# Kernel tuning notes

Measured on AMD Instinct MI355X. Metric: run time of the kernel, lower is better.

The kernel has to match this reference:

```python
import jax, jax.numpy as jnp
import numpy as np

B, C, H, W = 4, 512, 32, 32
NH = 8
HD = C // NH
PH, PW = 2, 4
NPR = PH * PW
HIDDEN = int(C * 2.0)
EPS = 1e-5

def _bn(x, p):
    g, b, m, v = p[0], p[1], p[2], p[3]
    s = g * jax.lax.rsqrt(v + EPS)
    return x * s[None, :, None, None] + (b - m * s)[None, :, None, None]

def _ln(x, p):
    mu = x.mean(-1, keepdims=True)
    var = ((x - mu) ** 2).mean(-1, keepdims=True)
    return (x - mu) * jax.lax.rsqrt(var + EPS) * p[0] + p[1]

def _dwconv(x, w):
    return jax.lax.conv_general_dilated(
        x, w, (1, 1), 'SAME',
        dimension_numbers=('NCHW', 'OIHW', 'NCHW'),
        feature_group_count=x.shape[1])

def _pw(x, w):
    # 1x1 conv, no bias: w is (O, I, 1, 1)
    return jnp.einsum('bchw,oc->bohw', x, w[:, :, 0, 0])

def _pool(x, ph, pw):
    # adaptive avg pool when output evenly divides input
    b, c, h, w = x.shape
    return x.reshape(b, c, ph, h // ph, pw, w // pw).mean(axis=(3, 5))

def _gelu(x):
    return jax.nn.gelu(x, approximate=False)

def _coords(h, w):
    y = jnp.linspace(0.0, 1.0, h)
    x = jnp.linspace(0.0, 1.0, w)
    gy, gx = jnp.meshgrid(y, x, indexing='ij')
    return jnp.stack([gy, gx], axis=-1).reshape(-1, 2)


def setup_inputs() -> dict:
    key = jax.random.key(0)
    ks = iter(jax.random.split(key, 64))
    def nrm(shape, s=0.02):
        return jax.random.normal(next(ks), shape, jnp.float32) * s
    def bnp():
        return jnp.stack([1.0 + nrm((C,), 0.1), nrm((C,), 0.1),
                          nrm((C,), 0.1), 1.0 + jnp.abs(nrm((C,), 0.2))])
    def lnp(c=C):
        return jnp.stack([jnp.ones((c,), jnp.float32), jnp.zeros((c,), jnp.float32)])
    return {
        'fused': jax.random.normal(next(ks), (B, C, H, W), jnp.float32),
        'depth': jax.random.normal(next(ks), (B, C, H, W), jnp.float32),
        'pg_dw_w': nrm((C, 1, 3, 3)), 'pg_bn1': bnp(),
        'pg_pw_w': nrm((C, C, 1, 1)), 'pg_bn2': bnp(),
        'prompt_embed': nrm((1, NPR, C)), 'pg_ln': lnp(),
        'gp_dw_w': nrm((C, 1, 3, 3)), 'gp_bn': bnp(),
        'gp_pw_w': nrm((1, C, 1, 1)), 'gp_pw_b': jnp.zeros((1,), jnp.float32),
        'gp_weight': jnp.ones((2, 1, 1, 1), jnp.float32),
        'ln1': lnp(),
        'wq': nrm((C, C)), 'wk': nrm((C, C)), 'wv': nrm((C, C)), 'wo': nrm((C, C)),
        'ln2': lnp(),
        'mlp_w1': nrm((HIDDEN, C)), 'mlp_b1': jnp.zeros((HIDDEN,), jnp.float32),
        'mlp_w2': nrm((C, HIDDEN)), 'mlp_b2': jnp.zeros((C,), jnp.float32),
        'op_dw_w': nrm((C, 1, 3, 3)), 'op_bn1': bnp(),
        'op_pw_w': nrm((C, C, 1, 1)), 'op_bn2': bnp(),
    }


def reference(fused, depth, pg_dw_w, pg_bn1, pg_pw_w, pg_bn2, prompt_embed, pg_ln,
              gp_dw_w, gp_bn, gp_pw_w, gp_pw_b, gp_weight,
              ln1, wq, wk, wv, wo, ln2, mlp_w1, mlp_b1, mlp_w2, mlp_b2,
              op_dw_w, op_bn1, op_pw_w, op_bn2):
    b = fused.shape[0]
    # --- DepthPromptGenerator ---
    pp = _gelu(_bn(_dwconv(depth, pg_dw_w), pg_bn1))
    pp = _gelu(_bn(_pw(pp, pg_pw_w), pg_bn2))
    prompt = _pool(pp, PH, PW).reshape(b, C, NPR).transpose(0, 2, 1)  # (B, P, C)
    prompt = _ln(prompt + prompt_embed, pg_ln)
    # --- GeometryPriorGenerator ---
    ds = _gelu(_bn(_dwconv(depth, gp_dw_w), gp_bn))
    ds = _pw(ds, gp_pw_w) + gp_pw_b[None, :, None, None]  # (B,1,H,W)
    img_d = ds.reshape(b, H * W)
    pr_d = _pool(ds, PH, PW).reshape(b, NPR)
    jd = jnp.concatenate([pr_d, img_d], axis=1)  # (B, N) depth scalar per token
    coords = jnp.concatenate([_coords(PH, PW), _coords(H, W)], axis=0)  # (N,2)
    pos = jnp.abs(coords[:, None, :] - coords[None, :, :]).sum(-1)  # (N,N) L1 distance
    decay = jnp.log(1.0 - 2.0 ** (-1.0 - 4.0 * jnp.arange(NH, dtype=jnp.float32) / NH))
    pos_mask = pos[None, :, :] * decay[:, None, None]  # (NH,N,N)
    depth_mask = jnp.abs(jd[:, :, None] - jd[:, None, :])[:, None, :, :] * decay[None, :, None, None]
    bias = gp_weight[0, 0, 0, 0] * pos_mask[None] + gp_weight[1, 0, 0, 0] * depth_mask  # (B,NH,N,N)
    # --- GeometryAwarePromptMixer ---
    img_tok = fused.reshape(b, C, H * W).transpose(0, 2, 1)  # (B,HW,C)
    jt = jnp.concatenate([prompt, img_tok], axis=1)  # (B,N,C)
    n = jt.shape[1]
    x = _ln(jt, ln1)
    q = jnp.einsum('bnc,dc->bnd', x, wq).reshape(b, n, NH, HD).transpose(0, 2, 1, 3)
    k = jnp.einsum('bnc,dc->bnd', x, wk).reshape(b, n, NH, HD).transpose(0, 2, 1, 3)
    v = jnp.einsum('bnc,dc->bnd', x, wv).reshape(b, n, NH, HD).transpose(0, 2, 1, 3)
    logits = jnp.einsum('bhnd,bhmd->bhnm', q, k) * (HD ** -0.5) + bias
    attn = jax.nn.softmax(logits, axis=-1)
    ao = jnp.einsum('bhnm,bhmd->bhnd', attn, v).transpose(0, 2, 1, 3).reshape(b, n, C)
    jt = jt + jnp.einsum('bnc,dc->bnd', ao, wo)
    h = _gelu(jnp.einsum('bnc,hc->bnh', _ln(jt, ln2), mlp_w1) + mlp_b1)
    jt = jt + jnp.einsum('bnh,ch->bnc', h, mlp_w2) + mlp_b2
    enh = jt[:, NPR:, :].transpose(0, 2, 1).reshape(b, C, H, W)
    # --- out_proj ---
    o = _gelu(_bn(_dwconv(enh, op_dw_w), op_bn1))
    o = _bn(_pw(o, op_pw_w), op_bn2)
    return fused + o
```

## Files before the change

### kernel.cpp

```cpp
#include <hip/hip_runtime.h>
#include <math.h>

typedef __attribute__((ext_vector_type(8))) short bf16x8;
typedef __attribute__((ext_vector_type(4))) float f32x4;

#define CH 512
#define HWP 1024
#define NTOK 1032
#define NTP 1088
#define NPRM 8
#define BB 4
#define EPSV 1e-5f
#define MTOK 4128
#define MPAD 4224
#define QSCL 0.18033688f
#define LOG2E 1.44269504f

__device__ __forceinline__ float gelu_f(float x) {
  return 0.5f * x * (1.0f + erff(x * 0.70710678118654752440f));
}

__device__ __forceinline__ ushort f2bf(float x) {
  union { float f; unsigned u; } v; v.f = x;
  unsigned r = v.u + 0x7FFF + ((v.u >> 16) & 1);
  return (ushort)(r >> 16);
}

__device__ __forceinline__ float bf2f(ushort u) {
  union { unsigned u; float f; } v; v.u = ((unsigned)u) << 16;
  return v.f;
}

__device__ __forceinline__ void gl16(const ushort* g, ushort* s) {
  __builtin_amdgcn_global_load_lds(
      (const __attribute__((address_space(1))) unsigned int*)g,
      (__attribute__((address_space(3))) unsigned int*)s,
      16, 0, 0);
}

__global__ __launch_bounds__(256) void convw(
    const float* __restrict__ wq, const float* __restrict__ wk, const float* __restrict__ wv,
    const float* __restrict__ wo, const float* __restrict__ w1, const float* __restrict__ w2,
    const float* __restrict__ pgw, const float* __restrict__ opw, const float* __restrict__ gpw,
    ushort* __restrict__ out)
{
  const int total = 2621952;
  for (int i = blockIdx.x * 256 + threadIdx.x; i < total; i += gridDim.x * 256) {
    const float* src; int off;
    if (i < 262144)       { src = wq;  off = i; }
    else if (i < 524288)  { src = wk;  off = i - 262144; }
    else if (i < 786432)  { src = wv;  off = i - 524288; }
    else if (i < 1048576) { src = wo;  off = i - 786432; }
    else if (i < 1572864) { src = w1;  off = i - 1048576; }
    else if (i < 2097152) { src = w2;  off = i - 1572864; }
    else if (i < 2359296) { src = pgw; off = i - 2097152; }
    else if (i < 2621440) { src = opw; off = i - 2359296; }
    else                  { src = gpw; off = i - 2621440; }
    out[i] = f2bf(src[off]);
  }
}

__global__ __launch_bounds__(256) void dwt_dual(
    const float* __restrict__ in,
    const float* __restrict__ w1p, const float* __restrict__ bn1,
    const float* __restrict__ w2p, const float* __restrict__ bn2,
    ushort* __restrict__ o1, ushort* __restrict__ o2)
{
  __shared__ float t1[32][33];
  __shared__ float t2[32][33];
  const int y = blockIdx.x;
  const int c0 = blockIdx.y * 32;
  const int b = blockIdx.z;
  const int tx = threadIdx.x, ty = threadIdx.y;
  #pragma unroll
  for (int i = 0; i < 4; ++i) {
    int c = c0 + ty + i * 8;
    const float* ip = in + ((size_t)(b * CH + c)) * HWP;
    const float* wa = w1p + c * 9;
    const float* wb = w2p + c * 9;
    float a1 = 0.0f, a2 = 0.0f;
    #pragma unroll
    for (int dy = 0; dy < 3; ++dy) {
      int yy = y + dy - 1;
      if ((unsigned)yy < 32u) {
        #pragma unroll
        for (int dx = 0; dx < 3; ++dx) {
          int xx = tx + dx - 1;
          if ((unsigned)xx < 32u) {
            float v = ip[yy * 32 + xx];
            a1 += v * wa[dy * 3 + dx];
            a2 += v * wb[dy * 3 + dx];
          }
        }
      }
    }
    float g1 = bn1[c], be1 = bn1[CH + c], m1 = bn1[2 * CH + c], v1 = bn1[3 * CH + c];
    float s1 = g1 * rsqrtf(v1 + EPSV);
    t1[ty + i * 8][tx] = gelu_f(a1 * s1 + (be1 - m1 * s1));
    float g2 = bn2[c], be2 = bn2[CH + c], m2 = bn2[2 * CH + c], v2 = bn2[3 * CH + c];
    float s2 = g2 * rsqrtf(v2 + EPSV);
    t2[ty + i * 8][tx] = gelu_f(a2 * s2 + (be2 - m2 * s2));
  }
  __syncthreads();
  #pragma unroll
  for (int i = 0; i < 4; ++i) {
    size_t row = (size_t)(b * HWP + y * 32 + ty + i * 8) * CH + c0 + tx;
    o1[row] = f2bf(t1[tx][ty + i * 8]);
    o2[row] = f2bf(t2[tx][ty + i * 8]);
  }
}

template<int KH>
__device__ __forceinline__ void g64_core(
    const ushort* __restrict__ Ab, const ushort* __restrict__ Bb,
    int KA, int KB, ushort* sA, ushort* sB,
    f32x4 (&acc)[2][2], int l, int w)
{
  const int wr = (w >> 1) * 32, wc = (w & 1) * 32;
  #pragma unroll
  for (int kh = 0; kh < KH; ++kh) {
    if (kh) __syncthreads();
    #pragma unroll
    for (int j = 0; j < 8; ++j) {
      int r2 = w * 16 + j * 2;
      int row = r2 + (l >> 5);
      int chk = (l & 31) ^ (row & 7);
      gl16(Ab + (size_t)row * KA + kh * 256 + chk * 8, sA + r2 * 256);
      gl16(Bb + (size_t)row * KB + kh * 256 + chk * 8, sB + r2 * 256);
    }
    __syncthreads();
    #pragma unroll
    for (int kt = 0; kt < 8; ++kt) {
      int q = kt * 4 + (l >> 4);
      int r0 = wr + (l & 15), r1 = wr + 16 + (l & 15);
      int c0i = wc + (l & 15), c1i = wc + 16 + (l & 15);
      bf16x8 a0 = *(const bf16x8*)(sA + r0 * 256 + ((q ^ (r0 & 7)) * 8));
      bf16x8 a1 = *(const bf16x8*)(sA + r1 * 256 + ((q ^ (r1 & 7)) * 8));
      bf16x8 b0 = *(const bf16x8*)(sB + c0i * 256 + ((q ^ (c0i & 7)) * 8));
      bf16x8 b1 = *(const bf16x8*)(sB + c1i * 256 + ((q ^ (c1i & 7)) * 8));
      acc[0][0] = __builtin_amdgcn_mfma_f32_16x16x32_bf16(a0, b0, acc[0][0], 0, 0, 0);
      acc[0][1] = __builtin_amdgcn_mfma_f32_16x16x32_bf16(a0, b1, acc[0][1], 0, 0, 0);
      acc[1][0] = __builtin_amdgcn_mfma_f32_16x16x32_bf16(a1, b0, acc[1][0], 0, 0, 0);
      acc[1][1] = __builtin_amdgcn_mfma_f32_16x16x32_bf16(a1, b1, acc[1][1], 0, 0, 0);
    }
  }
}

#define G64_PRE(Abase, Bbase, KAv, KBv, KHv) \
  __shared__ ushort sA[16384], sB[16384]; \
  f32x4 acc[2][2]; \
  { f32x4 z = {0.f, 0.f, 0.f, 0.f}; acc[0][0] = z; acc[0][1] = z; acc[1][0] = z; acc[1][1] = z; } \
  const int l = threadIdx.x & 63, w = threadIdx.x >> 6; \
  const int wr = (w >> 1) * 32, wc = (w & 1) * 32; \
  g64_core<KHv>((Abase), (Bbase), (KAv), (KBv), sA, sB, acc, l, w);

__global__ __launch_bounds__(256) void g_qkv(
    const ushort* __restrict__ A, const ushort* __restrict__ B,
    ushort* __restrict__ qh, ushort* __restrict__ kh, ushort* __restrict__ vt)
{
  const int n0 = blockIdx.x * 64, m0 = blockIdx.y * 64;
  G64_PRE(A + (size_t)m0 * 512, B + (size_t)n0 * 512, 512, 512, 2)
  #pragma unroll
  for (int nf = 0; nf < 2; ++nf) {
    int n = n0 + wc + nf * 16 + (l & 15);
    #pragma unroll
    for (int mf = 0; mf < 2; ++mf) {
      #pragma unroll
      for (int r = 0; r < 4; ++r) {
        int m = m0 + wr + mf * 16 + (l >> 4) * 4 + r;
        if (m < MTOK) {
          int b = m / NTOK;
          int tok = m - b * NTOK;
          float val = acc[mf][nf][r];
          if (n < 512) {
            qh[((size_t)((b * 8 + (n >> 6)) * NTP) + tok) * 64 + (n & 63)] = f2bf(val * QSCL);
          } else if (n < 1024) {
            int n2 = n - 512;
            kh[((size_t)((b * 8 + (n2 >> 6)) * NTP) + tok) * 64 + (n2 & 63)] = f2bf(val);
          } else {
            int n2 = n - 1024;
            vt[((size_t)((b * 8 + (n2 >> 6)) * 64) + (n2 & 63)) * NTP + tok] = f2bf(val);
          }
        }
      }
    }
  }
}

template<int KH>
__global__ __launch_bounds__(256) void g_res(
    const ushort* __restrict__ A, const ushort* __restrict__ B,
    float* __restrict__ Cf, const float* __restrict__ bias)
{
  const int n0 = blockIdx.x * 64, m0 = blockIdx.y * 64;
  G64_PRE(A + (size_t)m0 * (KH * 256), B + (size_t)n0 * (KH * 256), KH * 256, KH * 256, KH)
  #pragma unroll
  for (int nf = 0; nf < 2; ++nf) {
    int n = n0 + wc + nf * 16 + (l & 15);
    float bv = bias ? bias[n] : 0.0f;
    #pragma unroll
    for (int mf = 0; mf < 2; ++mf) {
      #pragma unroll
      for (int r = 0; r < 4; ++r) {
        int m = m0 + wr + mf * 16 + (l >> 4) * 4 + r;
        if (m < MTOK) Cf[(size_t)m * 512 + n] += acc[mf][nf][r] + bv;
      }
    }
  }
}

__global__ __launch_bounds__(256) void g_gelu(
    const ushort* __restrict__ A, const ushort* __restrict__ B,
    const float* __restrict__ bias, ushort* __restrict__ Ob)
{
  const int n0 = blockIdx.x * 64, m0 = blockIdx.y * 64;
  G64_PRE(A + (size_t)m0 * 512, B + (size_t)n0 * 512, 512, 512, 2)
  #pragma unroll
  for (int nf = 0; nf < 2; ++nf) {
    int n = n0 + wc + nf * 16 + (l & 15);
    float bv = bias[n];
    #pragma unroll
    for (int mf = 0; mf < 2; ++mf) {
      #pragma unroll
      for (int r = 0; r < 4; ++r) {
        int m = m0 + wr + mf * 16 + (l >> 4) * 4 + r;
        if (m < MTOK) Ob[(size_t)m * 1024 + n] = f2bf(gelu_f(acc[mf][nf][r] + bv));
      }
    }
  }
}

__global__ __launch_bounds__(256) void g_pw_pool(
    const ushort* __restrict__ A, const ushort* __restrict__ B,
    const float* __restrict__ bnp, float* __restrict__ ppool)
{
  __shared__ float poolL[8][64];
  const int hw0 = blockIdx.x * 64, m0 = blockIdx.y * 64;
  const int b = blockIdx.z;
  {
    int t = threadIdx.x;
    #pragma unroll
    for (int k = 0; k < 2; ++k) { int idx = t + k * 256; poolL[idx >> 6][idx & 63] = 0.0f; }
  }
  G64_PRE(A + (size_t)m0 * 512, B + (size_t)(b * HWP + hw0) * 512, 512, 512, 2)
  __syncthreads();
  #pragma unroll
  for (int mf = 0; mf < 2; ++mf) {
    #pragma unroll
    for (int r = 0; r < 4; ++r) {
      int ol = wr + mf * 16 + (l >> 4) * 4 + r;
      int o = m0 + ol;
      float g = bnp[o], be = bnp[CH + o], mm = bnp[2 * CH + o], vv = bnp[3 * CH + o];
      float s = g * rsqrtf(vv + EPSV);
      float sh = be - mm * s;
      #pragma unroll
      for (int nf = 0; nf < 2; ++nf) {
        int hw = hw0 + wc + nf * 16 + (l & 15);
        float x = gelu_f(acc[mf][nf][r] * s + sh);
        int y = hw >> 5, xx = hw & 31;
        int rg = (y >> 4) * 4 + (xx >> 3);
        atomicAdd(&poolL[rg][ol], x);
      }
    }
  }
  __syncthreads();
  {
    int t = threadIdx.x;
    #pragma unroll
    for (int k = 0; k < 2; ++k) {
      int idx = t + k * 256;
      int rg = idx >> 6, oo = idx & 63;
      float v = poolL[rg][oo];
      if (v != 0.0f)
        atomicAdd(&ppool[((size_t)(b * 8 + rg)) * 512 + m0 + oo], v * (1.0f / 128.0f));
    }
  }
}

__global__ __launch_bounds__(256) void g_pw_res(
    const ushort* __restrict__ A, const ushort* __restrict__ B,
    const float* __restrict__ bnp, const float* __restrict__ res, float* __restrict__ Of)
{
  const int hw0 = blockIdx.x * 64, m0 = blockIdx.y * 64;
  const int b = blockIdx.z;
  G64_PRE(A + (size_t)m0 * 512, B + (size_t)(b * HWP + hw0) * 512, 512, 512, 2)
  #pragma unroll
  for (int mf = 0; mf < 2; ++mf) {
    #pragma unroll
    for (int r = 0; r < 4; ++r) {
      int o = m0 + wr + mf * 16 + (l >> 4) * 4 + r;
      float g = bnp[o], be = bnp[CH + o], mm = bnp[2 * CH + o], vv = bnp[3 * CH + o];
      float s = g * rsqrtf(vv + EPSV);
      float sh = be - mm * s;
      #pragma unroll
      for (int nf = 0; nf < 2; ++nf) {
        int hw = hw0 + wc + nf * 16 + (l & 15);
        size_t oi = ((size_t)(b * CH + o)) * HWP + hw;
        Of[oi] = acc[mf][nf][r] * s + sh + res[oi];
      }
    }
  }
}

__global__ __launch_bounds__(256) void combo_mid(
    const float* __restrict__ fused, const float* __restrict__ ppool,
    const float* __restrict__ embed, const float* __restrict__ pgln,
    const float* __restrict__ ln1, float* __restrict__ jt, ushort* __restrict__ xb,
    const ushort* __restrict__ dwT2, const ushort* __restrict__ gpw,
    const float* __restrict__ b0, float* __restrict__ jdv)
{
  __shared__ float T[32][513];
  __shared__ float red[16];
  const int t = threadIdx.x;
  const int bx = blockIdx.x;
  if (bx < 128) {
    int b = bx >> 5, hw0 = (bx & 31) * 32;
    int tx = t & 31, ty = t >> 5;
    #pragma unroll
    for (int cc = 0; cc < 512; cc += 8)
      T[tx][cc + ty] = fused[((size_t)(b * 512 + cc + ty)) * 1024 + hw0 + tx];
    __syncthreads();
    int tok = t >> 3, j = t & 7;
    float s = 0.f, sq = 0.f;
    #pragma unroll
    for (int i = 0; i < 64; ++i) {
      float v = T[tok][j * 64 + i];
      s += v; sq += v * v;
    }
    s += __shfl_xor(s, 1); sq += __shfl_xor(sq, 1);
    s += __shfl_xor(s, 2); sq += __shfl_xor(sq, 2);
    s += __shfl_xor(s, 4); sq += __shfl_xor(sq, 4);
    float mu = s * (1.f / 512.f);
    float var = sq * (1.f / 512.f) - mu * mu;
    float rstd = rsqrtf(var + EPSV);
    size_t row = (size_t)(b * NTOK + NPRM + hw0 + tok);
    #pragma unroll
    for (int i = 0; i < 64; i += 4) {
      int c = j * 64 + i;
      float4 v4;
      v4.x = T[tok][c]; v4.y = T[tok][c + 1]; v4.z = T[tok][c + 2]; v4.w = T[tok][c + 3];
      *(float4*)(jt + row * 512 + c) = v4;
      ushort4 u;
      u.x = f2bf((v4.x - mu) * rstd * ln1[c] + ln1[512 + c]);
      u.y = f2bf((v4.y - mu) * rstd * ln1[c + 1] + ln1[512 + c + 1]);
      u.z = f2bf((v4.z - mu) * rstd * ln1[c + 2] + ln1[512 + c + 2]);
      u.w = f2bf((v4.w - mu) * rstd * ln1[c + 3] + ln1[512 + c + 3]);
      *(ushort4*)(xb + row * 512 + c) = u;
    }
  } else if (bx < 160) {
    int idx = bx - 128, b = idx >> 3, pI = idx & 7;
    int c = t * 2;
    float2 v = *(const float2*)(ppool + ((size_t)(b * 8 + pI)) * 512 + c);
    float2 e = *(const float2*)(embed + pI * 512 + c);
    v.x += e.x; v.y += e.y;
    float s = v.x + v.y, sq = v.x * v.x + v.y * v.y;
    #pragma unroll
    for (int off = 1; off < 64; off <<= 1) { s += __shfl_xor(s, off); sq += __shfl_xor(sq, off); }
    if ((t & 63) == 0) { red[(t >> 6) * 2] = s; red[(t >> 6) * 2 + 1] = sq; }
    __syncthreads();
    s = red[0] + red[2] + red[4] + red[6];
    sq = red[1] + red[3] + red[5] + red[7];
    float mu = s * (1.f / 512.f);
    float rstd = rsqrtf(sq * (1.f / 512.f) - mu * mu + EPSV);
    float o0 = (v.x - mu) * rstd * pgln[c] + pgln[512 + c];
    float o1 = (v.y - mu) * rstd * pgln[c + 1] + pgln[512 + c + 1];
    size_t row = (size_t)(b * NTOK + pI);
    jt[row * 512 + c] = o0;
    jt[row * 512 + c + 1] = o1;
    float s2 = o0 + o1, sq2 = o0 * o0 + o1 * o1;
    #pragma unroll
    for (int off = 1; off < 64; off <<= 1) { s2 += __shfl_xor(s2, off); sq2 += __shfl_xor(sq2, off); }
    if ((t & 63) == 0) { red[8 + (t >> 6) * 2] = s2; red[9 + (t >> 6) * 2] = sq2; }
    __syncthreads();
    s2 = red[8] + red[10] + red[12] + red[14];
    sq2 = red[9] + red[11] + red[13] + red[15];
    float mu2 = s2 * (1.f / 512.f);
    float rstd2 = rsqrtf(sq2 * (1.f / 512.f) - mu2 * mu2 + EPSV);
    xb[row * 512 + c]     = f2bf((o0 - mu2) * rstd2 * ln1[c] + ln1[512 + c]);
    xb[row * 512 + c + 1] = f2bf((o1 - mu2) * rstd2 * ln1[c + 1] + ln1[512 + c + 1]);
  } else {
    int idx = bx - 160;
    int b = idx >> 6, row0 = (idx & 63) * 16;
    int l = t & 63, w = t >> 6;
    bf16x8 wv = *(const bf16x8*)(gpw + l * 8);
    float wf[8];
    #pragma unroll
    for (int j = 0; j < 8; ++j) wf[j] = bf2f((ushort)wv[j]);
    float bias0 = b0[0];
    #pragma unroll
    for (int rr = 0; rr < 4; ++rr) {
      int hw = row0 + w * 4 + rr;
      bf16x8 xv = *(const bf16x8*)(dwT2 + ((size_t)(b * HWP + hw)) * CH + l * 8);
      float s = 0.0f;
      #pragma unroll
      for (int j = 0; j < 8; ++j) s += wf[j] * bf2f((ushort)xv[j]);
      #pragma unroll
      for (int off = 1; off < 64; off <<= 1) s += __shfl_xor(s, off);
      if (l == 0) {
        float sf = s + bias0;
        jdv[b * NTP + NPRM + hw] = sf;
        int y = hw >> 5, xx = hw & 31;
        int rg = (y >> 4) * 4 + (xx >> 3);
        atomicAdd(&jdv[b * NTP + rg], sf * (1.0f / 128.0f));
      }
    }
  }
}

__global__ __launch_bounds__(128) void ln_rows_bf(
    const float* __restrict__ in, const float* __restrict__ lnp, ushort* __restrict__ out)
{
  int row = blockIdx.x;
  float4 val = ((const float4*)(in + (size_t)row * CH))[threadIdx.x];
  float sum = val.x + val.y + val.z + val.w;
  float sq = val.x * val.x + val.y * val.y + val.z * val.z + val.w * val.w;
  #pragma unroll
  for (int off = 1; off < 64; off <<= 1) { sum += __shfl_xor(sum, off); sq += __shfl_xor(sq, off); }
  __shared__ float s2[4];
  if ((threadIdx.x & 63) == 0) { s2[(threadIdx.x >> 6) * 2] = sum; s2[(threadIdx.x >> 6) * 2 + 1] = sq; }
  __syncthreads();
  sum = s2[0] + s2[2]; sq = s2[1] + s2[3];
  float mu = sum * (1.0f / 512.0f);
  float var = sq * (1.0f / 512.0f) - mu * mu;
  float rstd = rsqrtf(var + EPSV);
  int c = threadIdx.x * 4;
  ushort4 o;
  o.x = f2bf((val.x - mu) * rstd * lnp[c] + lnp[CH + c]);
  o.y = f2bf((val.y - mu) * rstd * lnp[c + 1] + lnp[CH + c + 1]);
  o.z = f2bf((val.z - mu) * rstd * lnp[c + 2] + lnp[CH + c + 2]);
  o.w = f2bf((val.w - mu) * rstd * lnp[c + 3] + lnp[CH + c + 3]);
  *(ushort4*)(out + (size_t)row * CH + c) = o;
}

__global__ __launch_bounds__(256) void dwt_op(
    const float* __restrict__ jt, const float* __restrict__ w9p,
    const float* __restrict__ bn, ushort* __restrict__ outT)
{
  __shared__ float Tt[3][32][33];
  const int y = blockIdx.x;
  const int c0 = blockIdx.y * 32;
  const int b = blockIdx.z;
  const int tx = threadIdx.x, ty = threadIdx.y;
  #pragma unroll
  for (int ry = 0; ry < 3; ++ry) {
    int yy = y - 1 + ry;
    bool ok = (unsigned)yy < 32u;
    #pragma unroll
    for (int it = 0; it < 4; ++it) {
      int px = ty + it * 8;
      float v = ok ? jt[((size_t)(b * NTOK + NPRM + yy * 32 + px)) * 512 + c0 + tx] : 0.0f;
      Tt[ry][px][tx] = v;
    }
  }
  __syncthreads();
  int c = c0 + tx;
  float w9[9];
  #pragma unroll
  for (int k = 0; k < 9; ++k) w9[k] = w9p[c * 9 + k];
  float g = bn[c], be = bn[CH + c], mm = bn[2 * CH + c], vv = bn[3 * CH + c];
  float s = g * rsqrtf(vv + EPSV);
  float sh = be - mm * s;
  #pragma unroll
  for (int it = 0; it < 4; ++it) {
    int px = ty + it * 8;
    float acc = 0.0f;
    #pragma unroll
    for (int dy = 0; dy < 3; ++dy) {
      #pragma unroll
      for (int dx = 0; dx < 3; ++dx) {
        int xx = px + dx - 1;
        if ((unsigned)xx < 32u) acc += Tt[dy][xx][tx] * w9[dy * 3 + dx];
      }
    }
    outT[((size_t)(b * HWP + y * 32 + px)) * CH + c] = f2bf(gelu_f(acc * s + sh));
  }
}

__device__ __forceinline__ void tok_coord(int idx, float& y, float& x)
{
  if (idx < NPRM) { y = (float)(idx >> 2); x = (float)(idx & 3) * (1.0f / 3.0f); }
  else { int t = idx - NPRM; y = (float)(t >> 5) * (1.0f / 31.0f); x = (float)(t & 31) * (1.0f / 31.0f); }
}

__global__ __launch_bounds__(256) void attn_mfma3(
    const ushort* __restrict__ qh, const ushort* __restrict__ kh,
    const ushort* __restrict__ vT, const float* __restrict__ jd,
    const float* __restrict__ gw, ushort* __restrict__ ao)
{
  __shared__ ushort sK[8192], sV[8192];
  __shared__ ushort Pl[4][16][72];
  __shared__ float jdL[NTP];
  const int t = threadIdx.x, l = t & 63, w = t >> 6;
  const int h = blockIdx.y, b = blockIdx.z;
  const int i0 = blockIdx.x * 64 + w * 16;
  const ushort* Q = qh + (size_t)(b * 8 + h) * NTP * 64;
  const ushort* K = kh + (size_t)(b * 8 + h) * NTP * 64;
  const ushort* V = vT + (size_t)(b * 8 + h) * 64 * NTP;
  const float decay = logf(1.0f - exp2f(-1.0f - 0.5f * (float)h)) * LOG2E;
  const float g0 = gw[0] * decay, g1 = gw[1] * decay;

  for (int i = t; i < NTP; i += 256) jdL[i] = jd[b * NTP + i];

  bf16x8 qf0 = *(const bf16x8*)(Q + (size_t)(i0 + (l & 15)) * 64 + (l >> 4) * 8);
  bf16x8 qf1 = *(const bf16x8*)(Q + (size_t)(i0 + (l & 15)) * 64 + 32 + (l >> 4) * 8);

  bf16x8 ones;
  {
    short ov = (short)((l & 15) == 0 ? 0x3F80 : 0);
    #pragma unroll
    for (int j = 0; j < 8; ++j) ones[j] = ov;
  }

  f32x4 of[4], lacc;
  { f32x4 z = {0.f, 0.f, 0.f, 0.f};
    #pragma unroll
    for (int d = 0; d < 4; ++d) of[d] = z;
    lacc = z; }

#define ASTAGE(buf, j0s) { \
    const ushort* gk = K + (size_t)((j0s) + l) * 64; \
    const ushort* gv = V + (size_t)l * NTP + (j0s); \
    gl16(gk + w * 8,       sK + (buf) * 4096 + w * 512); \
    gl16(gk + (w + 4) * 8, sK + (buf) * 4096 + (w + 4) * 512); \
    gl16(gv + w * 8,       sV + (buf) * 4096 + w * 512); \
    gl16(gv + (w + 4) * 8, sV + (buf) * 4096 + (w + 4) * 512); }

  ASTAGE(0, 0)
  __syncthreads();

  float yi[4], xi[4], jdi[4];
  #pragma unroll
  for (int r = 0; r < 4; ++r) {
    int i = i0 + (l >> 4) * 4 + r;
    tok_coord(i, yi[r], xi[r]);
    jdi[r] = jdL[i];
  }

  const int NJT = 17;
  for (int jti = 0; jti < NJT; ++jti) {
    const int j0 = jti * 64;
    if (jti + 1 < NJT) ASTAGE((jti + 1) & 1, j0 + 64)
    const ushort* bK = sK + (jti & 1) * 4096;
    const ushort* bV = sV + (jti & 1) * 4096;

    f32x4 sfr[4];
    __builtin_amdgcn_s_setprio(1);
    #pragma unroll
    for (int jf = 0; jf < 4; ++jf) {
      bf16x8 k0 = *(const bf16x8*)(bK + (((l >> 4)) * 64 + jf * 16 + (l & 15)) * 8);
      bf16x8 k1 = *(const bf16x8*)(bK + ((4 + (l >> 4)) * 64 + jf * 16 + (l & 15)) * 8);
      f32x4 z = {0.f, 0.f, 0.f, 0.f};
      z = __builtin_amdgcn_mfma_f32_16x16x32_bf16(qf0, k0, z, 0, 0, 0);
      z = __builtin_amdgcn_mfma_f32_16x16x32_bf16(qf1, k1, z, 0, 0, 0);
      sfr[jf] = z;
    }
    __builtin_amdgcn_s_setprio(0);
    #pragma unroll
    for (int jf = 0; jf < 4; ++jf) {
      int jj = j0 + jf * 16 + (l & 15);
      float yj, xj;
      tok_coord(jj, yj, xj);
      float jdj = jdL[jj];
      bool valid = jj < NTOK;
      #pragma unroll
      for (int r = 0; r < 4; ++r) {
        float bias = g0 * (fabsf(yi[r] - yj) + fabsf(xi[r] - xj)) + g1 * fabsf(jdi[r] - jdj);
        float p = valid ? exp2f(sfr[jf][r] + bias - 4.0f) : 0.0f;
        Pl[w][(l >> 4) * 4 + r][jf * 16 + (l & 15)] = f2bf(p);
      }
    }
    asm volatile("s_waitcnt lgkmcnt(0)" ::: "memory");
    bf16x8 pa0 = *(const bf16x8*)&Pl[w][l & 15][(l >> 4) * 8];
    bf16x8 pa1 = *(const bf16x8*)&Pl[w][l & 15][32 + (l >> 4) * 8];
    __builtin_amdgcn_s_setprio(1);
    #pragma unroll
    for (int df = 0; df < 4; ++df) {
      bf16x8 v0 = *(const bf16x8*)(bV + (((l >> 4)) * 64 + df * 16 + (l & 15)) * 8);
      bf16x8 v1 = *(const bf16x8*)(bV + ((4 + (l >> 4)) * 64 + df * 16 + (l & 15)) * 8);
      of[df] = __builtin_amdgcn_mfma_f32_16x16x32_bf16(pa0, v0, of[df], 0, 0, 0);
      of[df] = __builtin_amdgcn_mfma_f32_16x16x32_bf16(pa1, v1, of[df], 0, 0, 0);
    }
    lacc = __builtin_amdgcn_mfma_f32_16x16x32_bf16(pa0, ones, lacc, 0, 0, 0);
    lacc = __builtin_amdgcn_mfma_f32_16x16x32_bf16(pa1, ones, lacc, 0, 0, 0);
    __builtin_amdgcn_s_setprio(0);
    __syncthreads();
  }
  #pragma unroll
  for (int r = 0; r < 4; ++r) {
    int i = i0 + (l >> 4) * 4 + r;
    float lsum = __shfl(lacc[r], (l & 48), 64);
    if (i < NTOK) {
      float inv = 1.0f / lsum;
      #pragma unroll
      for (int df = 0; df < 4; ++df)
        ao[((size_t)(b * NTOK + i)) * 512 + h * 64 + df * 16 + (l & 15)] = f2bf(of[df][r] * inv);
    }
  }
}

extern "C" void kernel_launch(void* const* d_in, const int* in_sizes, int n_in,
                              void* d_out, int out_size, void* d_ws, size_t ws_size,
                              hipStream_t stream)
{
  const float* fused = (const float*)d_in[0];
  const float* depth = (const float*)d_in[1];
  const float* pg_dw_w = (const float*)d_in[2];
  const float* pg_bn1 = (const float*)d_in[3];
  const float* pg_pw_w = (const float*)d_in[4];
  const float* pg_bn2 = (const float*)d_in[5];
  const float* prompt_embed = (const float*)d_in[6];
  const float* pg_ln = (const float*)d_in[7];
  const float* gp_dw_w = (const float*)d_in[8];
  const float* gp_bn = (const float*)d_in[9];
  const float* gp_pw_w = (const float*)d_in[10];
  const float* gp_pw_b = (const float*)d_in[11];
  const float* gp_weight = (const float*)d_in[12];
  const float* ln1 = (const float*)d_in[13];
  const float* wq = (const float*)d_in[14];
  const float* wk = (const float*)d_in[15];
  const float* wv = (const float*)d_in[16];
  const float* wo = (const float*)d_in[17];
  const float* ln2 = (const float*)d_in[18];
  const float* mlp_w1 = (const float*)d_in[19];
  const float* mlp_b1 = (const float*)d_in[20];
  const float* mlp_w2 = (const float*)d_in[21];
  const float* mlp_b2 = (const float*)d_in[22];
  const float* op_dw_w = (const float*)d_in[23];
  const float* op_bn1 = (const float*)d_in[24];
  const float* op_pw_w = (const float*)d_in[25];
  const float* op_bn2 = (const float*)d_in[26];
  float* out = (float*)d_out;

  char* p = (char*)d_ws;
  auto alloc = [&](size_t bytes) { char* r = p; p += (bytes + 1023) & ~(size_t)1023; return r; };
  float*  jdv   = (float*) alloc((size_t)BB * NTP * 4);
  float*  ppool = (float*) alloc((size_t)BB * 8 * CH * 4);
  float*  jt    = (float*) alloc((size_t)MTOK * 512 * 4);
  ushort* xb    = (ushort*)alloc((size_t)MPAD * 512 * 2);
  ushort* hb    = (ushort*)alloc((size_t)MPAD * 1024 * 2);
  ushort* ao    = (ushort*)alloc((size_t)MPAD * 512 * 2);
  ushort* qhB   = (ushort*)alloc((size_t)32 * NTP * 64 * 2);
  ushort* khB   = (ushort*)alloc((size_t)32 * NTP * 64 * 2);
  ushort* vTB   = (ushort*)alloc((size_t)32 * NTP * 64 * 2);
  ushort* dwT1  = (ushort*)alloc((size_t)BB * HWP * CH * 2);
  ushort* dwT2  = (ushort*)alloc((size_t)BB * HWP * CH * 2);
  ushort* wbf   = (ushort*)alloc((size_t)2621952 * 2);

  ushort* wqkv_bf = wbf;
  ushort* wo_bf   = wbf + 786432;
  ushort* w1_bf   = wbf + 1048576;
  ushort* w2_bf   = wbf + 1572864;
  ushort* pgw_bf  = wbf + 2097152;
  ushort* opw_bf  = wbf + 2359296;
  ushort* gpw_bf  = wbf + 2621440;

  hipMemsetAsync(jdv, 0, (size_t)BB * NTP * 4, stream);
  hipMemsetAsync(ppool, 0, (size_t)BB * 8 * CH * 4, stream);

  hipLaunchKernelGGL(convw, dim3(2048), dim3(256), 0, stream,
                     wq, wk, wv, wo, mlp_w1, mlp_w2, pg_pw_w, op_pw_w, gp_pw_w, wbf);

  hipLaunchKernelGGL(dwt_dual, dim3(32, 16, BB), dim3(32, 8), 0, stream,
                     depth, pg_dw_w, pg_bn1, gp_dw_w, gp_bn, dwT1, dwT2);
  hipLaunchKernelGGL(g_pw_pool, dim3(16, 8, BB), dim3(256), 0, stream, pgw_bf, dwT1, pg_bn2, ppool);
  hipLaunchKernelGGL(combo_mid, dim3(416), dim3(256), 0, stream,
                     fused, ppool, prompt_embed, pg_ln, ln1, jt, xb, dwT2, gpw_bf, gp_pw_b, jdv);
  hipLaunchKernelGGL(g_qkv, dim3(24, 65), dim3(256), 0, stream, xb, wqkv_bf, qhB, khB, vTB);
  hipLaunchKernelGGL(attn_mfma3, dim3(17, 8, BB), dim3(256), 0, stream, qhB, khB, vTB, jdv, gp_weight, ao);
  hipLaunchKernelGGL(g_res<2>, dim3(8, 65), dim3(256), 0, stream, ao, wo_bf, jt, (const float*)nullptr);
  hipLaunchKernelGGL(ln_rows_bf, dim3(MTOK), dim3(128), 0, stream, jt, ln2, xb);
  hipLaunchKernelGGL(g_gelu, dim3(16, 65), dim3(256), 0, stream, xb, w1_bf, mlp_b1, hb);
  hipLaunchKernelGGL(g_res<4>, dim3(8, 65), dim3(256), 0, stream, hb, w2_bf, jt, mlp_b2);
  hipLaunchKernelGGL(dwt_op, dim3(32, 16, BB), dim3(32, 8), 0, stream, jt, op_dw_w, op_bn1, dwT1);
  hipLaunchKernelGGL(g_pw_res, dim3(16, 8, BB), dim3(256), 0, stream, opw_bf, dwT1, op_bn2, fused, out);
}
```

Before: 331.6 us.

## Widen attention blocks to 128 queries, swizzle K/V LDS, split V transpose

The attention kernel now runs 512 threads per block covering 128 query rows, so each staged K/V tile is shared by twice as many waves. The K/V shared-memory layout is XOR-swizzled to avoid LDS bank conflicts, and the per-batch depth values are read from global memory instead of an LDS copy. The QKV GEMM now writes V in row-major head layout with coalesced stores, and a separate tiled transpose kernel produces V transposed. The token padding grows to a multiple of 128 to fit the new tiling. The cost is an extra launch, an extra V buffer and a round trip through memory for V.

```diff
diff --git a/kernel.cpp b/kernel.cpp
--- a/kernel.cpp
+++ b/kernel.cpp
@@ -7,7 +7,7 @@
 #define CH 512
 #define HWP 1024
 #define NTOK 1032
-#define NTP 1088
+#define NTP 1152
 #define NPRM 8
 #define BB 4
 #define EPSV 1e-5f
@@ -156,13 +156,16 @@
 
 __global__ __launch_bounds__(256) void g_qkv(
     const ushort* __restrict__ A, const ushort* __restrict__ B,
-    ushort* __restrict__ qh, ushort* __restrict__ kh, ushort* __restrict__ vt)
+    ushort* __restrict__ qh, ushort* __restrict__ kh, ushort* __restrict__ vh)
 {
   const int n0 = blockIdx.x * 64, m0 = blockIdx.y * 64;
   G64_PRE(A + (size_t)m0 * 512, B + (size_t)n0 * 512, 512, 512, 2)
   #pragma unroll
   for (int nf = 0; nf < 2; ++nf) {
     int n = n0 + wc + nf * 16 + (l & 15);
+    ushort* dst = (n < 512) ? qh : (n < 1024 ? kh : vh);
+    int n2 = n & 511;
+    float scl = (n < 512) ? QSCL : 1.0f;
     #pragma unroll
     for (int mf = 0; mf < 2; ++mf) {
       #pragma unroll
@@ -171,20 +174,26 @@
         if (m < MTOK) {
           int b = m / NTOK;
           int tok = m - b * NTOK;
-          float val = acc[mf][nf][r];
-          if (n < 512) {
-            qh[((size_t)((b * 8 + (n >> 6)) * NTP) + tok) * 64 + (n & 63)] = f2bf(val * QSCL);
-          } else if (n < 1024) {
-            int n2 = n - 512;
-            kh[((size_t)((b * 8 + (n2 >> 6)) * NTP) + tok) * 64 + (n2 & 63)] = f2bf(val);
-          } else {
-            int n2 = n - 1024;
-            vt[((size_t)((b * 8 + (n2 >> 6)) * 64) + (n2 & 63)) * NTP + tok] = f2bf(val);
-          }
+          dst[((size_t)((b * 8 + (n2 >> 6)) * NTP) + tok) * 64 + (n2 & 63)] = f2bf(acc[mf][nf][r] * scl);
         }
       }
     }
   }
+}
+
+__global__ __launch_bounds__(256) void transp_v(const ushort* __restrict__ vh, ushort* __restrict__ vT)
+{
+  __shared__ ushort tile[32][33];
+  int tok0 = blockIdx.x * 32, d0 = blockIdx.y * 32;
+  int bh = blockIdx.z;
+  int tx = threadIdx.x, ty = threadIdx.y;
+  #pragma unroll
+  for (int i = 0; i < 4; ++i)
+    tile[ty + i * 8][tx] = vh[((size_t)bh * NTP + tok0 + ty + i * 8) * 64 + d0 + tx];
+  __syncthreads();
+  #pragma unroll
+  for (int i = 0; i < 4; ++i)
+    vT[((size_t)bh * 64 + d0 + ty + i * 8) * NTP + tok0 + tx] = tile[tx][ty + i * 8];
 }
 
 template<int KH>
@@ -482,24 +491,22 @@
   else { int t = idx - NPRM; y = (float)(t >> 5) * (1.0f / 31.0f); x = (float)(t & 31) * (1.0f / 31.0f); }
 }
 
-__global__ __launch_bounds__(256) void attn_mfma3(
+__global__ __launch_bounds__(512) void attn_mfma4(
     const ushort* __restrict__ qh, const ushort* __restrict__ kh,
     const ushort* __restrict__ vT, const float* __restrict__ jd,
     const float* __restrict__ gw, ushort* __restrict__ ao)
 {
   __shared__ ushort sK[8192], sV[8192];
-  __shared__ ushort Pl[4][16][72];
-  __shared__ float jdL[NTP];
+  __shared__ ushort Pl[8][16][72];
   const int t = threadIdx.x, l = t & 63, w = t >> 6;
   const int h = blockIdx.y, b = blockIdx.z;
-  const int i0 = blockIdx.x * 64 + w * 16;
+  const int i0 = blockIdx.x * 128 + w * 16;
   const ushort* Q = qh + (size_t)(b * 8 + h) * NTP * 64;
   const ushort* K = kh + (size_t)(b * 8 + h) * NTP * 64;
   const ushort* V = vT + (size_t)(b * 8 + h) * 64 * NTP;
+  const float* jdb = jd + b * NTP;
   const float decay = logf(1.0f - exp2f(-1.0f - 0.5f * (float)h)) * LOG2E;
   const float g0 = gw[0] * decay, g1 = gw[1] * decay;
-
-  for (int i = t; i < NTP; i += 256) jdL[i] = jd[b * NTP + i];
 
   bf16x8 qf0 = *(const bf16x8*)(Q + (size_t)(i0 + (l & 15)) * 64 + (l >> 4) * 8);
   bf16x8 qf1 = *(const bf16x8*)(Q + (size_t)(i0 + (l & 15)) * 64 + 32 + (l >> 4) * 8);
@@ -518,12 +525,10 @@
     lacc = z; }
 
 #define ASTAGE(buf, j0s) { \
-    const ushort* gk = K + (size_t)((j0s) + l) * 64; \
-    const ushort* gv = V + (size_t)l * NTP + (j0s); \
-    gl16(gk + w * 8,       sK + (buf) * 4096 + w * 512); \
-    gl16(gk + (w + 4) * 8, sK + (buf) * 4096 + (w + 4) * 512); \
-    gl16(gv + w * 8,       sV + (buf) * 4096 + w * 512); \
-    gl16(gv + (w + 4) * 8, sV + (buf) * 4096 + (w + 4) * 512); }
+    int srow = w * 8 + (l >> 3); \
+    int schk = (l & 7) ^ (srow & 7); \
+    gl16(K + (size_t)((j0s) + srow) * 64 + schk * 8, sK + (buf) * 4096 + w * 512); \
+    gl16(V + (size_t)srow * NTP + (j0s) + schk * 8, sV + (buf) * 4096 + w * 512); }
 
   ASTAGE(0, 0)
   __syncthreads();
@@ -533,7 +538,7 @@
   for (int r = 0; r < 4; ++r) {
     int i = i0 + (l >> 4) * 4 + r;
     tok_coord(i, yi[r], xi[r]);
-    jdi[r] = jdL[i];
+    jdi[r] = jdb[i];
   }
 
   const int NJT = 17;
@@ -547,8 +552,9 @@
     __builtin_amdgcn_s_setprio(1);
     #pragma unroll
     for (int jf = 0; jf < 4; ++jf) {
-      bf16x8 k0 = *(const bf16x8*)(bK + (((l >> 4)) * 64 + jf * 16 + (l & 15)) * 8);
-      bf16x8 k1 = *(const bf16x8*)(bK + ((4 + (l >> 4)) * 64 + jf * 16 + (l & 15)) * 8);
+      int kr = jf * 16 + (l & 15);
+      bf16x8 k0 = *(const bf16x8*)(bK + kr * 64 + (((l >> 4) ^ (kr & 7)) * 8));
+      bf16x8 k1 = *(const bf16x8*)(bK + kr * 64 + (((4 + (l >> 4)) ^ (kr & 7)) * 8));
       f32x4 z = {0.f, 0.f, 0.f, 0.f};
       z = __builtin_amdgcn_mfma_f32_16x16x32_bf16(qf0, k0, z, 0, 0, 0);
       z = __builtin_amdgcn_mfma_f32_16x16x32_bf16(qf1, k1, z, 0, 0, 0);
@@ -560,7 +566,7 @@
       int jj = j0 + jf * 16 + (l & 15);
       float yj, xj;
       tok_coord(jj, yj, xj);
-      float jdj = jdL[jj];
+      float jdj = jdb[jj];
       bool valid = jj < NTOK;
       #pragma unroll
       for (int r = 0; r < 4; ++r) {
@@ -575,8 +581,9 @@
     __builtin_amdgcn_s_setprio(1);
     #pragma unroll
     for (int df = 0; df < 4; ++df) {
-      bf16x8 v0 = *(const bf16x8*)(bV + (((l >> 4)) * 64 + df * 16 + (l & 15)) * 8);
-      bf16x8 v1 = *(const bf16x8*)(bV + ((4 + (l >> 4)) * 64 + df * 16 + (l & 15)) * 8);
+      int vr = df * 16 + (l & 15);
+      bf16x8 v0 = *(const bf16x8*)(bV + vr * 64 + (((l >> 4) ^ (vr & 7)) * 8));
+      bf16x8 v1 = *(const bf16x8*)(bV + vr * 64 + (((4 + (l >> 4)) ^ (vr & 7)) * 8));
       of[df] = __builtin_amdgcn_mfma_f32_16x16x32_bf16(pa0, v0, of[df], 0, 0, 0);
       of[df] = __builtin_amdgcn_mfma_f32_16x16x32_bf16(pa1, v1, of[df], 0, 0, 0);
     }
@@ -641,6 +648,7 @@
   ushort* ao    = (ushort*)alloc((size_t)MPAD * 512 * 2);
   ushort* qhB   = (ushort*)alloc((size_t)32 * NTP * 64 * 2);
   ushort* khB   = (ushort*)alloc((size_t)32 * NTP * 64 * 2);
+  ushort* vhB   = (ushort*)alloc((size_t)32 * NTP * 64 * 2);
   ushort* vTB   = (ushort*)alloc((size_t)32 * NTP * 64 * 2);
   ushort* dwT1  = (ushort*)alloc((size_t)BB * HWP * CH * 2);
   ushort* dwT2  = (ushort*)alloc((size_t)BB * HWP * CH * 2);
@@ -665,8 +673,9 @@
   hipLaunchKernelGGL(g_pw_pool, dim3(16, 8, BB), dim3(256), 0, stream, pgw_bf, dwT1, pg_bn2, ppool);
   hipLaunchKernelGGL(combo_mid, dim3(416), dim3(256), 0, stream,
                      fused, ppool, prompt_embed, pg_ln, ln1, jt, xb, dwT2, gpw_bf, gp_pw_b, jdv);
-  hipLaunchKernelGGL(g_qkv, dim3(24, 65), dim3(256), 0, stream, xb, wqkv_bf, qhB, khB, vTB);
-  hipLaunchKernelGGL(attn_mfma3, dim3(17, 8, BB), dim3(256), 0, stream, qhB, khB, vTB, jdv, gp_weight, ao);
+  hipLaunchKernelGGL(g_qkv, dim3(24, 65), dim3(256), 0, stream, xb, wqkv_bf, qhB, khB, vhB);
+  hipLaunchKernelGGL(transp_v, dim3(36, 2, 32), dim3(32, 8), 0, stream, vhB, vTB);
+  hipLaunchKernelGGL(attn_mfma4, dim3(9, 8, BB), dim3(512), 0, stream, qhB, khB, vTB, jdv, gp_weight, ao);
   hipLaunchKernelGGL(g_res<2>, dim3(8, 65), dim3(256), 0, stream, ao, wo_bf, jt, (const float*)nullptr);
   hipLaunchKernelGGL(ln_rows_bf, dim3(MTOK), dim3(128), 0, stream, jt, ln2, xb);
   hipLaunchKernelGGL(g_gelu, dim3(16, 65), dim3(256), 0, stream, xb, w1_bf, mlp_b1, hb);
```

Measured after the change: 331.6 us. About the same (-0.0%).
